# Performance work log

Hardware: AMD Instinct MI355X
Metric: run time of the kernel (lower is better)

## Reference

```python
import jax, jax.numpy as jnp
import numpy as np

E = 8        # num experts
TOPK = 2
H = 1024     # hidden size
F = 4096     # ffn hidden size
SL, BS = 2048, 2
TOKENS = SL * BS
N = TOKENS * TOPK          # flattened routing assignments
CAP = (TOPK * TOKENS) // E # expert_capacity with capacity_factor=1.0


def setup_inputs() -> dict:
    key = jax.random.key(0)
    ks = jax.random.split(key, 6)
    x = jax.random.normal(ks[0], (SL, BS, H), jnp.float32)
    scores = jax.random.uniform(ks[1], (TOKENS, E), dtype=jnp.float32)
    expert_weights = jax.random.uniform(ks[2], (TOKENS, TOPK), dtype=jnp.float32)
    top_experts = jax.random.randint(ks[3], (TOKENS, TOPK), 0, E, dtype=jnp.int32)
    w1 = jax.random.normal(ks[4], (E, H, F), jnp.float32) * 0.02
    w2 = jax.random.normal(ks[5], (E, F, H), jnp.float32) * 0.02
    bias = jnp.zeros((H,), jnp.float32)
    return {"x": x, "scores": scores, "expert_weights": expert_weights,
            "top_experts": top_experts, "w1": w1, "w2": w2, "bias": bias}


def reference(x, scores, expert_weights, top_experts, w1, w2, bias):
    # --- indices_and_bins: stable sort tokens by expert, histogram, cumsum ---
    te = top_experts.reshape(-1)          # [N] int
    ew = expert_weights.reshape(-1)       # [N]
    xf = x.reshape(-1, H)                 # [TOKENS, H]

    indices = jnp.argsort(te)             # stable sort -> permutation [N]
    bin_ids = te[indices]                 # sorted expert ids [N]
    tpe = jax.ops.segment_sum(jnp.ones_like(te), te, num_segments=E)  # tokens per expert
    bins = jnp.cumsum(tpe)                # inclusive cumsum
    starts = bins - tpe                   # start offset of each expert's bin
    pos = jnp.arange(N) - starts[bin_ids] # position within expert bin [N]
    valid = pos < CAP                     # capacity drop mask
    tok = indices // TOPK                 # source token row for each assignment

    # --- binned_gather: [E, CAP, H], zero padded, tokens beyond capacity dropped ---
    dst = jnp.where(valid, pos, CAP)      # out-of-range -> dropped via mode='drop'
    buf = jnp.zeros((E, CAP, H), x.dtype).at[bin_ids, dst].set(xf[tok], mode='drop')

    # --- grouped MLP: per-expert gelu FFN ---
    h = jax.nn.gelu(jnp.einsum('ech,ehf->ecf', buf, w1), approximate=False)
    y = jnp.einsum('ecf,efh->ech', h, w2)

    # --- binned_scatter: weighted un-permute back to token order ---
    vals = y[bin_ids, jnp.where(valid, pos, 0)]                      # [N, H]
    w = jnp.where(valid, ew[indices], 0.0)[:, None]
    out = jnp.zeros((TOKENS, H), x.dtype).at[tok].add(vals * w)

    return out.reshape(x.shape) + bias
```

## Files before the change

kernel.cpp:

```cpp
#include <hip/hip_runtime.h>
#include <hip/hip_bf16.h>
#include <math.h>

#define NE 8
#define TOPK 2
#define HD 1024
#define FD 4096
#define NTOK 4096
#define NASSIGN 8192
#define CAP 1024

typedef __attribute__((ext_vector_type(8))) short short8;
typedef __attribute__((ext_vector_type(4))) float f32x4;
typedef __attribute__((ext_vector_type(4))) unsigned short us4;
typedef __attribute__((ext_vector_type(4))) unsigned int u32x4;

__device__ __forceinline__ unsigned short f2bf(float f) {
  unsigned u = __float_as_uint(f);
  u += 0x7fffu + ((u >> 16) & 1u);
  return (unsigned short)(u >> 16);
}

__device__ __forceinline__ void load_lds16(const void* g, void* l) {
  __builtin_amdgcn_global_load_lds((const __attribute__((address_space(1))) void*)g,
                                   (__attribute__((address_space(3))) void*)l, 16, 0, 0);
}

__device__ __forceinline__ unsigned swz(unsigned b) {
  return b ^ (((b >> 7) & 3u) << 4);
}

__global__ __launch_bounds__(256)
void transpose_convert(const float* __restrict__ W, unsigned short* __restrict__ Wt,
                       int R, int C) {
  __shared__ float tile[64][65];
  int e = blockIdx.z;
  W  += (size_t)e * R * C;
  Wt += (size_t)e * R * C;
  int c0 = blockIdx.x * 64, r0 = blockIdx.y * 64;
  int tx = threadIdx.x & 15, ty = threadIdx.x >> 4;
#pragma unroll
  for (int i = 0; i < 4; ++i) {
    f32x4 v = *(const f32x4*)(W + (size_t)(r0 + ty + i * 16) * C + c0 + tx * 4);
    tile[ty + i * 16][tx * 4 + 0] = v.x;
    tile[ty + i * 16][tx * 4 + 1] = v.y;
    tile[ty + i * 16][tx * 4 + 2] = v.z;
    tile[ty + i * 16][tx * 4 + 3] = v.w;
  }
  __syncthreads();
#pragma unroll
  for (int i = 0; i < 4; ++i) {
    int c = ty + i * 16;
    us4 o;
    o.x = f2bf(tile[tx * 4 + 0][c]);
    o.y = f2bf(tile[tx * 4 + 1][c]);
    o.z = f2bf(tile[tx * 4 + 2][c]);
    o.w = f2bf(tile[tx * 4 + 3][c]);
    *(us4*)(Wt + (size_t)(c0 + c) * R + r0 + tx * 4) = o;
  }
}

__global__ __launch_bounds__(1024)
void routing_kernel(const int* __restrict__ te, int* __restrict__ rankA,
                    int* __restrict__ srcTok, int* __restrict__ counts) {
  __shared__ uint4 pref[1024];
  int t = threadIdx.x;
  int myTe[8];
  unsigned lc[4] = {0, 0, 0, 0};
#pragma unroll
  for (int j = 0; j < 8; ++j) {
    int ee = te[t * 8 + j];
    myTe[j] = ee;
    lc[ee >> 1] += 1u << ((ee & 1) * 16);
  }
  uint4 inc;
  inc.x = lc[0]; inc.y = lc[1]; inc.z = lc[2]; inc.w = lc[3];
  pref[t] = inc;
  __syncthreads();
  for (int d = 1; d < 1024; d <<= 1) {
    uint4 add;
    bool has = (t >= d);
    if (has) add = pref[t - d];
    __syncthreads();
    if (has) {
      inc.x += add.x; inc.y += add.y; inc.z += add.z; inc.w += add.w;
      pref[t] = inc;
    }
    __syncthreads();
  }
  uint4 tot = pref[1023];
  unsigned ex[4] = {inc.x - lc[0], inc.y - lc[1], inc.z - lc[2], inc.w - lc[3]};
  int run[8];
#pragma unroll
  for (int eidx = 0; eidx < 8; ++eidx)
    run[eidx] = (ex[eidx >> 1] >> ((eidx & 1) * 16)) & 0xffff;
#pragma unroll
  for (int j = 0; j < 8; ++j) {
    int ee = myTe[j];
    int r = run[ee]++;
    rankA[t * 8 + j] = r;
    if (r < CAP) srcTok[ee * CAP + r] = (t * 8 + j) >> 1;
  }
  if (t < 8) {
    unsigned tt[4] = {tot.x, tot.y, tot.z, tot.w};
    counts[t] = (tt[t >> 1] >> ((t & 1) * 16)) & 0xffff;
  }
}

__global__ __launch_bounds__(128)
void gather_kernel(const float* __restrict__ x, const int* __restrict__ srcTok,
                   const int* __restrict__ counts, unsigned short* __restrict__ buf) {
  int row = blockIdx.x;
  int e = row >> 10;
  int c = row & (CAP - 1);
  int t = threadIdx.x;
  unsigned short* dst = buf + (size_t)row * HD + t * 8;
  if (c < counts[e]) {
    const float* src = x + (size_t)srcTok[row] * HD + t * 8;
    f32x4 v0 = *(const f32x4*)src;
    f32x4 v1 = *(const f32x4*)(src + 4);
    u32x4 o;
    o.x = f2bf(v0.x) | ((unsigned)f2bf(v0.y) << 16);
    o.y = f2bf(v0.z) | ((unsigned)f2bf(v0.w) << 16);
    o.z = f2bf(v1.x) | ((unsigned)f2bf(v1.y) << 16);
    o.w = f2bf(v1.z) | ((unsigned)f2bf(v1.w) << 16);
    *(u32x4*)dst = o;
  } else {
    u32x4 z = {0, 0, 0, 0};
    *(u32x4*)dst = z;
  }
}

template <int KTOT, int NDIM, int DO_GELU, int KSPLIT>
__global__ __launch_bounds__(512, 2)
void gemm256(const unsigned short* __restrict__ Ab, const unsigned short* __restrict__ Bb,
             void* __restrict__ Cv) {
  constexpr int KLOC = KTOT / KSPLIT;
  constexpr int NT = KLOC / 32;
  constexpr int GX = CAP / 256;
  constexpr int GY = NDIM / 256;
  constexpr int NWG = GX * GY * NE * KSPLIT;
  __shared__ char smem[4 * 32768];

  int orig = blockIdx.x;
  int wg = (orig & 7) * (NWG / 8) + (orig >> 3);
  int bx = wg % GX;
  int by = (wg / GX) % GY;
  int zz = wg / (GX * GY);
  int ks = zz % KSPLIT;
  int e  = zz / KSPLIT;

  const unsigned short* A  = Ab + (size_t)e * CAP * KTOT;
  const unsigned short* Bt = Bb + (size_t)e * NDIM * KTOT;
  int bm = bx * 256, bn = by * 256;
  int kbase = ks * KLOC;

  int tid = threadIdx.x;
  int lane = tid & 63;
  int w = tid >> 6;
  int wr = w >> 2, wc = w & 3;
  int l15 = lane & 15, lq = lane >> 4;

  unsigned aoff[8], boff[4];
#pragma unroll
  for (int m = 0; m < 8; ++m)
    aoff[m] = swz((unsigned)((wr * 128 + m * 16 + l15) * 64 + lq * 16));
#pragma unroll
  for (int n = 0; n < 4; ++n)
    boff[n] = swz((unsigned)((wc * 64 + n * 16 + l15) * 64 + lq * 16));

  const char *srcA0, *srcA1, *srcB0, *srcB1;
  unsigned dA0, dA1, dB0, dB1;
  {
    int idx0 = tid, idx1 = 512 + tid;
    int r0_ = idx0 >> 2, r1_ = idx1 >> 2;
    unsigned kb0 = ((unsigned)(idx0 & 3) * 16) ^ ((((unsigned)r0_ >> 1) & 3u) << 4);
    unsigned kb1 = ((unsigned)(idx1 & 3) * 16) ^ ((((unsigned)r1_ >> 1) & 3u) << 4);
    srcA0 = (const char*)(A  + (size_t)(bm + r0_) * KTOT + kbase) + kb0;
    srcA1 = (const char*)(A  + (size_t)(bm + r1_) * KTOT + kbase) + kb1;
    srcB0 = (const char*)(Bt + (size_t)(bn + r0_) * KTOT + kbase) + kb0;
    srcB1 = (const char*)(Bt + (size_t)(bn + r1_) * KTOT + kbase) + kb1;
    dA0 = (unsigned)idx0 * 16; dA1 = (unsigned)idx1 * 16;
    dB0 = 16384u + (unsigned)idx0 * 16; dB1 = 16384u + (unsigned)idx1 * 16;
  }

#pragma unroll
  for (int tt = 0; tt < 3; ++tt) {
    char* db = smem + tt * 32768;
    load_lds16(srcA0 + tt * 64, db + dA0);
    load_lds16(srcA1 + tt * 64, db + dA1);
    load_lds16(srcB0 + tt * 64, db + dB0);
    load_lds16(srcB1 + tt * 64, db + dB1);
  }
  srcA0 += 192; srcA1 += 192; srcB0 += 192; srcB1 += 192;
  asm volatile("s_waitcnt vmcnt(4)" ::: "memory");
  __builtin_amdgcn_s_barrier();

  f32x4 acc[8][4] = {};
  short8 afLo0[4], afLo1[4], bf0[4], bf1[4], af47[4];

#pragma unroll
  for (int j = 0; j < 4; ++j) afLo0[j] = *(const short8*)(smem + aoff[j]);
#pragma unroll
  for (int n = 0; n < 4; ++n) bf0[n]  = *(const short8*)(smem + 16384 + boff[n]);

#define TILE(T, CUR, NXT)                                                         \
  {                                                                               \
    const int t_ = (T);                                                           \
    const char* rb_ = smem + (t_ & 3) * 32768;                                    \
    _Pragma("unroll") for (int j = 0; j < 4; ++j)                                 \
        af47[j] = *(const short8*)(rb_ + aoff[4 + j]);                            \
    if (t_ + 3 < NT) {                                                            \
      char* db_ = smem + ((t_ + 3) & 3) * 32768;                                  \
      load_lds16(srcA0, db_ + dA0);                                               \
      load_lds16(srcA1, db_ + dA1);                                               \
    }                                                                             \
    __builtin_amdgcn_sched_barrier(0);                                            \
    __builtin_amdgcn_s_setprio(1);                                                \
    _Pragma("unroll") for (int m = 0; m < 4; ++m)                                 \
      _Pragma("unroll") for (int n = 0; n < 4; ++n)                               \
        acc[m][n] = __builtin_amdgcn_mfma_f32_16x16x32_bf16(                      \
            afLo##CUR[m], bf##CUR[n], acc[m][n], 0, 0, 0);                        \
    __builtin_amdgcn_s_setprio(0);                                                \
    __builtin_amdgcn_sched_barrier(0);                                            \
    if (t_ + 1 < NT) {                                                            \
      const char* rn_ = smem + ((t_ + 1) & 3) * 32768;                            \
      _Pragma("unroll") for (int j = 0; j < 4; ++j)                               \
          afLo##NXT[j] = *(const short8*)(rn_ + aoff[j]);                         \
      _Pragma("unroll") for (int n = 0; n < 4; ++n)                               \
          bf##NXT[n] = *(const short8*)(rn_ + 16384 + boff[n]);                   \
    }                                                                             \
    if (t_ + 3 < NT) {                                                            \
      char* db_ = smem + ((t_ + 3) & 3) * 32768;                                  \
      load_lds16(srcB0, db_ + dB0);                                               \
      load_lds16(srcB1, db_ + dB1);                                               \
    }                                                                             \
    __builtin_amdgcn_sched_barrier(0);                                            \
    __builtin_amdgcn_s_setprio(1);                                                \
    _Pragma("unroll") for (int m = 0; m < 4; ++m)                                 \
      _Pragma("unroll") for (int n = 0; n < 4; ++n)                               \
        acc[m + 4][n] = __builtin_amdgcn_mfma_f32_16x16x32_bf16(                  \
            af47[m], bf##CUR[n], acc[m + 4][n], 0, 0, 0);                         \
    __builtin_amdgcn_s_setprio(0);                                                \
    __builtin_amdgcn_sched_barrier(0);                                            \
    asm volatile("s_waitcnt vmcnt(4)" ::: "memory");                              \
    __builtin_amdgcn_s_barrier();                                                 \
    srcA0 += 64; srcA1 += 64; srcB0 += 64; srcB1 += 64;                           \
  }

#pragma unroll 1
  for (int t = 0; t < NT; t += 2) {
    TILE(t, 0, 1);
    TILE(t + 1, 1, 0);
  }
#undef TILE

  int r0 = bm + wr * 128 + lq * 4;
  int c0 = bn + wc * 64 + l15;
  if (DO_GELU) {
    unsigned short* C = (unsigned short*)Cv + (size_t)e * CAP * NDIM;
#pragma unroll
    for (int m = 0; m < 8; ++m)
#pragma unroll
      for (int n = 0; n < 4; ++n)
#pragma unroll
        for (int j = 0; j < 4; ++j) {
          float v = acc[m][n][j];
          float y = 0.7978845608028654f * (v + 0.044715f * v * v * v);
          float g = v / (1.0f + __expf(-2.0f * y));
          C[(size_t)(r0 + m * 16 + j) * NDIM + (c0 + n * 16)] = f2bf(g);
        }
  } else {
    float* C = (float*)Cv + ((size_t)ks * NE + e) * CAP * NDIM;
#pragma unroll
    for (int m = 0; m < 8; ++m)
#pragma unroll
      for (int n = 0; n < 4; ++n)
#pragma unroll
        for (int j = 0; j < 4; ++j)
          C[(size_t)(r0 + m * 16 + j) * NDIM + (c0 + n * 16)] = acc[m][n][j];
  }
}

__global__ __launch_bounds__(128)
void scatter_kernel(const float* __restrict__ y, const int* __restrict__ te,
                    const int* __restrict__ rankA, const float* __restrict__ ew,
                    const float* __restrict__ bias, float* __restrict__ out) {
  int tk = blockIdx.x;
  int t = threadIdx.x;
  f32x4 a0 = *(const f32x4*)(bias + t * 8);
  f32x4 a1 = *(const f32x4*)(bias + t * 8 + 4);
#pragma unroll
  for (int k = 0; k < TOPK; ++k) {
    int a = tk * TOPK + k;
    int r = rankA[a];
    if (r < CAP) {
      float wgt = ew[a];
      size_t rowoff = ((size_t)te[a] * CAP + r) * HD + t * 8;
      const float* y0 = y + rowoff;
      const float* y1 = y + (size_t)NE * CAP * HD + rowoff;
      f32x4 v0 = *(const f32x4*)y0 + *(const f32x4*)y1;
      f32x4 v1 = *(const f32x4*)(y0 + 4) + *(const f32x4*)(y1 + 4);
      a0 += wgt * v0;
      a1 += wgt * v1;
    }
  }
  float* o = out + (size_t)tk * HD + t * 8;
  *(f32x4*)o = a0;
  *(f32x4*)(o + 4) = a1;
}

extern "C" void kernel_launch(void* const* d_in, const int* in_sizes, int n_in,
                              void* d_out, int out_size, void* d_ws, size_t ws_size,
                              hipStream_t stream) {
  const float* x    = (const float*)d_in[0];
  const float* ew   = (const float*)d_in[2];
  const int*   te   = (const int*)d_in[3];
  const float* w1   = (const float*)d_in[4];
  const float* w2   = (const float*)d_in[5];
  const float* bias = (const float*)d_in[6];
  float* out = (float*)d_out;

  unsigned short* w1t  = (unsigned short*)d_ws;
  unsigned short* w2t  = w1t + (size_t)NE * HD * FD;
  unsigned short* bufg = w2t + (size_t)NE * HD * FD;
  unsigned short* hbuf = bufg + (size_t)NE * CAP * HD;
  float*          ybuf = (float*)w1t;
  int* rankA  = (int*)(hbuf + (size_t)NE * CAP * FD);
  int* srcTok = rankA + NASSIGN;
  int* counts = srcTok + NE * CAP;

  transpose_convert<<<dim3(FD / 64, HD / 64, NE), 256, 0, stream>>>(w1, w1t, HD, FD);
  transpose_convert<<<dim3(HD / 64, FD / 64, NE), 256, 0, stream>>>(w2, w2t, FD, HD);
  routing_kernel<<<1, 1024, 0, stream>>>(te, rankA, srcTok, counts);
  gather_kernel<<<NE * CAP, 128, 0, stream>>>(x, srcTok, counts, bufg);
  gemm256<HD, FD, 1, 1><<<512, 512, 0, stream>>>(bufg, w1t, (void*)hbuf);
  gemm256<FD, HD, 0, 2><<<256, 512, 0, stream>>>(hbuf, w2t, (void*)ybuf);
  scatter_kernel<<<NTOK, 128, 0, stream>>>(ybuf, te, rankA, ew, bias, out);
}
```

Baseline: 258.0 us.

## Unroll GEMM main loop by four with static LDS offsets and merge weight transposes

The GEMM main loop is unrolled to four tiles per iteration, so the LDS buffer addresses and the global source offsets become compile-time immediates instead of per-tile computed swizzle arrays and pointer increments. This saves VGPRs and address arithmetic in the hot loop. The final tiles now wait with vmcnt(0) instead of vmcnt(4). The two weight transpose/convert kernels are merged into one launch, which removes one kernel launch and the gap between them. The unroll assumes NT is a multiple of four.

Measured after the change: 406.3 us. +57.5%, slower.

```diff
diff --git a/kernel.cpp b/kernel.cpp
--- a/kernel.cpp
+++ b/kernel.cpp
@@ -26,18 +26,22 @@
                                    (__attribute__((address_space(3))) void*)l, 16, 0, 0);
 }
 
-__device__ __forceinline__ unsigned swz(unsigned b) {
-  return b ^ (((b >> 7) & 3u) << 4);
-}
-
 __global__ __launch_bounds__(256)
-void transpose_convert(const float* __restrict__ W, unsigned short* __restrict__ Wt,
-                       int R, int C) {
+void transpose_both(const float* __restrict__ w1, const float* __restrict__ w2,
+                    unsigned short* __restrict__ w1t, unsigned short* __restrict__ w2t) {
   __shared__ float tile[64][65];
-  int e = blockIdx.z;
-  W  += (size_t)e * R * C;
-  Wt += (size_t)e * R * C;
-  int c0 = blockIdx.x * 64, r0 = blockIdx.y * 64;
+  int z = blockIdx.z;
+  const float* W;
+  unsigned short* Wt;
+  int R, C, c0, r0;
+  if (z < NE) {
+    W = w1 + (size_t)z * HD * FD; Wt = w1t + (size_t)z * HD * FD;
+    R = HD; C = FD; c0 = blockIdx.x * 64; r0 = blockIdx.y * 64;
+  } else {
+    int e = z - NE;
+    W = w2 + (size_t)e * HD * FD; Wt = w2t + (size_t)e * HD * FD;
+    R = FD; C = HD; c0 = blockIdx.y * 64; r0 = blockIdx.x * 64;
+  }
   int tx = threadIdx.x & 15, ty = threadIdx.x >> 4;
 #pragma unroll
   for (int i = 0; i < 4; ++i) {
@@ -88,8 +92,8 @@
     }
     __syncthreads();
   }
+  unsigned ex[4] = {inc.x - lc[0], inc.y - lc[1], inc.z - lc[2], inc.w - lc[3]};
   uint4 tot = pref[1023];
-  unsigned ex[4] = {inc.x - lc[0], inc.y - lc[1], inc.z - lc[2], inc.w - lc[3]};
   int run[8];
 #pragma unroll
   for (int eidx = 0; eidx < 8; ++eidx)
@@ -161,38 +165,34 @@
   int wr = w >> 2, wc = w & 3;
   int l15 = lane & 15, lq = lane >> 4;
 
-  unsigned aoff[8], boff[4];
-#pragma unroll
-  for (int m = 0; m < 8; ++m)
-    aoff[m] = swz((unsigned)((wr * 128 + m * 16 + l15) * 64 + lq * 16));
-#pragma unroll
-  for (int n = 0; n < 4; ++n)
-    boff[n] = swz((unsigned)((wc * 64 + n * 16 + l15) * 64 + lq * 16));
-
-  const char *srcA0, *srcA1, *srcB0, *srcB1;
-  unsigned dA0, dA1, dB0, dB1;
+  unsigned sw = (unsigned)((lq ^ ((l15 >> 1) & 3)) << 4);
+  const char* pA  = smem + (unsigned)((wr * 128 + l15) * 64) + sw;
+  const char* pA2 = pA + 65536;
+  const char* pB  = smem + 16384u + (unsigned)((wc * 64 + l15) * 64) + sw;
+  const char* pB2 = pB + 65536;
+
+  const char *sA0, *sA1, *sB0, *sB1;
+  char *dA0, *dA1, *dB0, *dB1;
   {
-    int idx0 = tid, idx1 = 512 + tid;
-    int r0_ = idx0 >> 2, r1_ = idx1 >> 2;
-    unsigned kb0 = ((unsigned)(idx0 & 3) * 16) ^ ((((unsigned)r0_ >> 1) & 3u) << 4);
-    unsigned kb1 = ((unsigned)(idx1 & 3) * 16) ^ ((((unsigned)r1_ >> 1) & 3u) << 4);
-    srcA0 = (const char*)(A  + (size_t)(bm + r0_) * KTOT + kbase) + kb0;
-    srcA1 = (const char*)(A  + (size_t)(bm + r1_) * KTOT + kbase) + kb1;
-    srcB0 = (const char*)(Bt + (size_t)(bn + r0_) * KTOT + kbase) + kb0;
-    srcB1 = (const char*)(Bt + (size_t)(bn + r1_) * KTOT + kbase) + kb1;
-    dA0 = (unsigned)idx0 * 16; dA1 = (unsigned)idx1 * 16;
-    dB0 = 16384u + (unsigned)idx0 * 16; dB1 = 16384u + (unsigned)idx1 * 16;
+    int i0 = tid, i1 = 512 + tid;
+    int r0_ = i0 >> 2, r1_ = i1 >> 2;
+    unsigned kb0 = ((unsigned)(i0 & 3) ^ (((unsigned)r0_ >> 1) & 3u)) << 4;
+    unsigned kb1 = ((unsigned)(i1 & 3) ^ (((unsigned)r1_ >> 1) & 3u)) << 4;
+    sA0 = (const char*)(A  + (size_t)(bm + r0_) * KTOT + kbase) + kb0;
+    sA1 = (const char*)(A  + (size_t)(bm + r1_) * KTOT + kbase) + kb1;
+    sB0 = (const char*)(Bt + (size_t)(bn + r0_) * KTOT + kbase) + kb0;
+    sB1 = (const char*)(Bt + (size_t)(bn + r1_) * KTOT + kbase) + kb1;
+    dA0 = smem + (unsigned)i0 * 16;  dA1 = smem + (unsigned)i1 * 16;
+    dB0 = smem + 16384u + (unsigned)i0 * 16; dB1 = smem + 16384u + (unsigned)i1 * 16;
   }
 
 #pragma unroll
   for (int tt = 0; tt < 3; ++tt) {
-    char* db = smem + tt * 32768;
-    load_lds16(srcA0 + tt * 64, db + dA0);
-    load_lds16(srcA1 + tt * 64, db + dA1);
-    load_lds16(srcB0 + tt * 64, db + dB0);
-    load_lds16(srcB1 + tt * 64, db + dB1);
-  }
-  srcA0 += 192; srcA1 += 192; srcB0 += 192; srcB1 += 192;
+    load_lds16(sA0 + tt * 64, dA0 + tt * 32768);
+    load_lds16(sA1 + tt * 64, dA1 + tt * 32768);
+    load_lds16(sB0 + tt * 64, dB0 + tt * 32768);
+    load_lds16(sB1 + tt * 64, dB1 + tt * 32768);
+  }
   asm volatile("s_waitcnt vmcnt(4)" ::: "memory");
   __builtin_amdgcn_s_barrier();
 
@@ -200,20 +200,18 @@
   short8 afLo0[4], afLo1[4], bf0[4], bf1[4], af47[4];
 
 #pragma unroll
-  for (int j = 0; j < 4; ++j) afLo0[j] = *(const short8*)(smem + aoff[j]);
-#pragma unroll
-  for (int n = 0; n < 4; ++n) bf0[n]  = *(const short8*)(smem + 16384 + boff[n]);
-
-#define TILE(T, CUR, NXT)                                                         \
+  for (int j = 0; j < 4; ++j) afLo0[j] = *(const short8*)(pA + j * 1024);
+#pragma unroll
+  for (int n = 0; n < 4; ++n) bf0[n]  = *(const short8*)(pB + n * 1024);
+
+#define TILE(U, CUR, NXT, PAc, OFFc, PAn, OFFn, PBc, PBn)                         \
   {                                                                               \
-    const int t_ = (T);                                                           \
-    const char* rb_ = smem + (t_ & 3) * 32768;                                    \
+    const int t_ = t + (U);                                                       \
     _Pragma("unroll") for (int j = 0; j < 4; ++j)                                 \
-        af47[j] = *(const short8*)(rb_ + aoff[4 + j]);                            \
+        af47[j] = *(const short8*)(PAc + (OFFc + (4 + j) * 1024));                \
     if (t_ + 3 < NT) {                                                            \
-      char* db_ = smem + ((t_ + 3) & 3) * 32768;                                  \
-      load_lds16(srcA0, db_ + dA0);                                               \
-      load_lds16(srcA1, db_ + dA1);                                               \
+      load_lds16(sA0 + ((U) + 3) * 64, dA0 + (((U) + 3) & 3) * 32768);            \
+      load_lds16(sA1 + ((U) + 3) * 64, dA1 + (((U) + 3) & 3) * 32768);            \
     }                                                                             \
     __builtin_amdgcn_sched_barrier(0);                                            \
     __builtin_amdgcn_s_setprio(1);                                                \
@@ -224,16 +222,14 @@
     __builtin_amdgcn_s_setprio(0);                                                \
     __builtin_amdgcn_sched_barrier(0);                                            \
     if (t_ + 1 < NT) {                                                            \
-      const char* rn_ = smem + ((t_ + 1) & 3) * 32768;                            \
       _Pragma("unroll") for (int j = 0; j < 4; ++j)                               \
-          afLo##NXT[j] = *(const short8*)(rn_ + aoff[j]);                         \
+          afLo##NXT[j] = *(const short8*)(PAn + (OFFn + j * 1024));               \
       _Pragma("unroll") for (int n = 0; n < 4; ++n)                               \
-          bf##NXT[n] = *(const short8*)(rn_ + 16384 + boff[n]);                   \
+          bf##NXT[n] = *(const short8*)(PBn + (OFFn + n * 1024));                 \
     }                                                                             \
     if (t_ + 3 < NT) {                                                            \
-      char* db_ = smem + ((t_ + 3) & 3) * 32768;                                  \
-      load_lds16(srcB0, db_ + dB0);                                               \
-      load_lds16(srcB1, db_ + dB1);                                               \
+      load_lds16(sB0 + ((U) + 3) * 64, dB0 + (((U) + 3) & 3) * 32768);            \
+      load_lds16(sB1 + ((U) + 3) * 64, dB1 + (((U) + 3) & 3) * 32768);            \
     }                                                                             \
     __builtin_amdgcn_sched_barrier(0);                                            \
     __builtin_amdgcn_s_setprio(1);                                                \
@@ -243,15 +239,18 @@
             af47[m], bf##CUR[n], acc[m + 4][n], 0, 0, 0);                         \
     __builtin_amdgcn_s_setprio(0);                                                \
     __builtin_amdgcn_sched_barrier(0);                                            \
-    asm volatile("s_waitcnt vmcnt(4)" ::: "memory");                              \
+    if (t_ + 3 < NT) asm volatile("s_waitcnt vmcnt(4)" ::: "memory");             \
+    else             asm volatile("s_waitcnt vmcnt(0)" ::: "memory");             \
     __builtin_amdgcn_s_barrier();                                                 \
-    srcA0 += 64; srcA1 += 64; srcB0 += 64; srcB1 += 64;                           \
   }
 
 #pragma unroll 1
-  for (int t = 0; t < NT; t += 2) {
-    TILE(t, 0, 1);
-    TILE(t + 1, 1, 0);
+  for (int t = 0; t < NT; t += 4) {
+    TILE(0, 0, 1, pA, 0, pA, 32768, pB, pB)
+    TILE(1, 1, 0, pA, 32768, pA2, 0, pB, pB2)
+    TILE(2, 0, 1, pA2, 0, pA2, 32768, pB2, pB2)
+    TILE(3, 1, 0, pA2, 32768, pA, 0, pB2, pB)
+    sA0 += 256; sA1 += 256; sB0 += 256; sB1 += 256;
   }
 #undef TILE
 
@@ -330,8 +329,7 @@
   int* srcTok = rankA + NASSIGN;
   int* counts = srcTok + NE * CAP;
 
-  transpose_convert<<<dim3(FD / 64, HD / 64, NE), 256, 0, stream>>>(w1, w1t, HD, FD);
-  transpose_convert<<<dim3(HD / 64, FD / 64, NE), 256, 0, stream>>>(w2, w2t, FD, HD);
+  transpose_both<<<dim3(FD / 64, HD / 64, NE * 2), 256, 0, stream>>>(w1, w2, w1t, w2t);
   routing_kernel<<<1, 1024, 0, stream>>>(te, rankA, srcTok, counts);
   gather_kernel<<<NE * CAP, 128, 0, stream>>>(x, srcTok, counts, bufg);
   gemm256<HD, FD, 1, 1><<<512, 512, 0, stream>>>(bufg, w1t, (void*)hbuf);
```
